# Kernel optimization log

Measured on AMD Instinct MI355X. Metric: run time of the kernel, lower is better.

The kernel has to match this reference:

```python
import jax, jax.numpy as jnp
import numpy as np
from functools import partial

V, H, B, T, L = 32000, 1024, 64, 64, 4
EOS = 2


def setup_inputs() -> dict:
    key = jax.random.key(0)
    ks = jax.random.split(key, 10)
    s = 1.0 / np.sqrt(H)
    return {
        "max_len": T,
        "tgt": jax.random.randint(ks[0], (B, T), 0, V),
        "h0": jax.random.normal(ks[1], (L, B, H), jnp.float32),
        "c0": jax.random.normal(ks[2], (L, B, H), jnp.float32),
        "embedding": jax.random.normal(ks[3], (V, H), jnp.float32) * s,
        "W_ih": jax.random.normal(ks[4], (L, 4 * H, H), jnp.float32) * s,
        "W_hh": jax.random.normal(ks[5], (L, 4 * H, H), jnp.float32) * s,
        "b_ih": jax.random.normal(ks[6], (L, 4 * H), jnp.float32) * s,
        "b_hh": jax.random.normal(ks[7], (L, 4 * H), jnp.float32) * s,
        "W_cls": jax.random.normal(ks[8], (V, H), jnp.float32) * s,
        "b_cls": jax.random.normal(ks[9], (V,), jnp.float32) * s,
    }


def _lstm_cell(x, h, c, Wi, Wh, bi, bh):
    # gates: [B, 4H] in torch order (i, f, g, o)
    g = x @ Wi.T + bi + h @ Wh.T + bh
    i, f, gg, o = jnp.split(g, 4, axis=-1)
    c2 = jax.nn.sigmoid(f) * c + jax.nn.sigmoid(i) * jnp.tanh(gg)
    h2 = jax.nn.sigmoid(o) * jnp.tanh(c2)
    return h2, c2


def reference(max_len, tgt, h0, c0, embedding, W_ih, W_hh, b_ih, b_hh, W_cls, b_cls):
    # step i>0 uses embedding of tgt[:, i-1].
    batch = tgt.shape[0]
    x0 = jnp.broadcast_to(embedding[EOS], (batch, embedding.shape[1]))
    tf_in = embedding[tgt[:, : max_len - 1]]              # [B, T-1, H]
    inputs = jnp.concatenate([x0[:, None, :], tf_in], axis=1)  # [B, T, H]
    inputs = jnp.swapaxes(inputs, 0, 1)                   # [T, B, H]

    def step(carry, x):
        h, c = carry  # each [L, B, H]
        hs, cs = [], []
        inp = x
        for l in range(L):  # 4 stacked LSTM cells, h of cell l feeds cell l+1
            hn, cn = _lstm_cell(inp, h[l], c[l], W_ih[l], W_hh[l], b_ih[l], b_hh[l])
            hs.append(hn)
            cs.append(cn)
            inp = hn
        h = jnp.stack(hs)
        c = jnp.stack(cs)
        logp = jax.nn.log_softmax(h[L - 1] @ W_cls.T + b_cls, axis=-1)  # [B, V]
        return (h, c), logp

    (h, c), out = jax.lax.scan(step, (h0, c0), inputs)
    return out, h, c  # out: [T, B, V]
```

## Files before the change

### kernel.cpp

```cpp
#include <hip/hip_runtime.h>

using u16 = unsigned short;
using u32 = unsigned int;

typedef __bf16 bf16x8 __attribute__((ext_vector_type(8)));
typedef float  f32x4  __attribute__((ext_vector_type(4)));
typedef u16    u16x8  __attribute__((ext_vector_type(8)));

static constexpr int kV = 32000, kH = 1024, kB = 64, kT = 64, kL = 4, kEOS = 2;

struct Flag { int v; int pad[15]; };

__device__ __forceinline__ u16 f2bf(float f) {
  u32 u = __float_as_uint(f);
  u = (u + 0x7fffu + ((u >> 16) & 1u)) >> 16;
  return (u16)u;
}
__device__ __forceinline__ float sigf(float x)   { return 1.0f / (1.0f + __expf(-x)); }
__device__ __forceinline__ float tanhf_(float x) { return 1.0f - 2.0f / (__expf(2.0f * x) + 1.0f); }

typedef const __attribute__((address_space(1))) u32* gas_ptr;
typedef __attribute__((address_space(3))) u32*       las_ptr;
__device__ __forceinline__ void async16(const u16* g, u16* l) {
  __builtin_amdgcn_global_load_lds((gas_ptr)g, (las_ptr)l, 16, 0, 0);
}

__device__ __forceinline__ void spin_ge(const int* p, int tgt) {
  while (__hip_atomic_load(p, __ATOMIC_RELAXED, __HIP_MEMORY_SCOPE_AGENT) < tgt)
    __builtin_amdgcn_s_sleep(2);
}

__device__ __forceinline__ size_t packed_off(int b, int k) {
  return (size_t)(((b >> 4) * 32 + (k >> 5)) * 512 + (((k >> 3) & 3) * 16 + (b & 15)) * 8 + (k & 7));
}

__device__ __forceinline__ u16x8 cvt8(const float* src) {
  const float4* s4 = (const float4*)src;
  float4 v0 = s4[0], v1 = s4[1];
  u16x8 r;
  r[0]=f2bf(v0.x); r[1]=f2bf(v0.y); r[2]=f2bf(v0.z); r[3]=f2bf(v0.w);
  r[4]=f2bf(v1.x); r[5]=f2bf(v1.y); r[6]=f2bf(v1.z); r[7]=f2bf(v1.w);
  return r;
}


__global__ void __launch_bounds__(256)
pack_lstm(const float* __restrict__ Wih, const float* __restrict__ Whh,
          u16* __restrict__ wpack) {
  __shared__ u16 lds[64 * 136];
  const int bid = blockIdx.x;
  const int lblk = bid >> 4, mt = (bid >> 3) & 1, kkg = bid & 7;
  const int lay = lblk >> 6, cb = lblk & 63;
  const int tid = threadIdx.x;
  const float* W = mt ? Whh : Wih;
  {
    const int rid = tid >> 2, q = tid & 3;
    const int gr = (rid >> 4) * 1024 + cb * 16 + (rid & 15);
    const float* src = W + ((size_t)lay * 4096 + gr) * 1024 + kkg * 128 + q * 32;
    u16* dst = lds + rid * 136 + q * 32;
    #pragma unroll
    for (int it = 0; it < 4; ++it)
      *(u16x8*)(dst + it * 8) = cvt8(src + it * 8);
  }
  __syncthreads();
  const int cf = tid >> 6, lane = tid & 63;
  const int rid = cf * 16 + (lane & 15);
  const int l4o = (lane >> 4) * 8;
  #pragma unroll
  for (int kl = 0; kl < 4; ++kl) {
    const int kk = kkg * 4 + kl;
    const u16x8 v = *(const u16x8*)(lds + rid * 136 + kl * 32 + l4o);
    *(u16x8*)(wpack + ((size_t)lblk * 16384 + mt * 8192 + kk * 256 + cf * 64 + lane) * 8) = v;
  }
}

__global__ void __launch_bounds__(256)
pack_cls(const float* __restrict__ W, u16* __restrict__ o) {
  __shared__ u16 lds[128 * 136];
  const int bid = blockIdx.x;
  const int bn = bid >> 3, kkg = bid & 7;
  const int tid = threadIdx.x;
  {
    const int row = tid >> 1, half = tid & 1;
    const float* src = W + ((size_t)(bn * 128 + row)) * 1024 + kkg * 128 + half * 64;
    u16* dst = lds + row * 136 + half * 64;
    #pragma unroll
    for (int it = 0; it < 8; ++it)
      *(u16x8*)(dst + it * 8) = cvt8(src + it * 8);
  }
  __syncthreads();
  #pragma unroll
  for (int kl = 0; kl < 4; ++kl) {
    const int kk = kkg * 4 + kl;
    #pragma unroll
    for (int q = 0; q < 2; ++q) {
      const int p = tid + q * 256, row = p & 127, l4 = p >> 7;
      const u16x8 v = *(const u16x8*)(lds + row * 136 + kl * 32 + l4 * 8);
      *(u16x8*)(o + ((size_t)bn * 16384 + kk * 512 + p) * 8) = v;
    }
  }
}

__global__ void pack_x(const float* __restrict__ emb, const int* __restrict__ tgt,
                       u16* __restrict__ X) {
  const int cid = blockIdx.x * 256 + threadIdx.x;
  const int kc = cid & 127, b = (cid >> 7) & 63, t = cid >> 13;
  const int tok = (t == 0) ? kEOS : tgt[b * 64 + t - 1];
  const u16x8 r = cvt8(emb + (size_t)tok * 1024 + kc * 8);
  *(u16x8*)(X + (size_t)t * 65536 + packed_off(b, kc * 8)) = r;
}

__global__ void pack_init(const float* __restrict__ h0, const float* __restrict__ bih,
                          const float* __restrict__ bhh, u16* __restrict__ hball,
                          float* __restrict__ bsum) {
  const int cid = blockIdx.x * 256 + threadIdx.x;
  if (cid < 32768) {
    const int kc = cid & 127, row = cid >> 7;
    const int lay = row >> 6, b = row & 63;
    const u16x8 r = cvt8(h0 + (size_t)cid * 8);
    *(u16x8*)(hball + (size_t)lay * 65 * 65536 + packed_off(b, kc * 8)) = r;
  } else {
    const int i = cid - 32768;
    bsum[i] = bih[i] + bhh[i];
  }
}

__global__ void __launch_bounds__(1024, 4)
lstm_coop(const u16* __restrict__ wpack, const u16* __restrict__ xall,
          u16* __restrict__ hball, const float* __restrict__ bsum,
          const float* __restrict__ c0, float* __restrict__ outh, float* __restrict__ outc,
          Flag* flags) {
  __shared__ u16 stg[3][32][512];
  __shared__ float Gc[2][64][80];

  const int tid = threadIdx.x, lane = tid & 63, wave = tid >> 6;
  const int l15 = lane & 15, l4 = lane >> 4;
  const int cmat = wave >> 3, cwc = (wave >> 1) & 3, ckh = wave & 1;
  const int blk = blockIdx.x;
  const int lay = (blk >> 1) & 3;
  const int cb  = ((blk >> 3) << 1) | (blk & 1);
  const int u0 = cb << 4;
  const int ub = tid >> 4, uu = tid & 15;

  float creg = c0[((size_t)lay * 64 + ub) * 1024 + u0 + uu];
  float bsv[4];
  #pragma unroll
  for (int g = 0; g < 4; ++g) bsv[g] = bsum[lay * 4096 + g * 1024 + u0 + uu];

  const size_t wbase = (size_t)(lay * 64 + cb) * 131072;
  bf16x8 breg[16];
  #pragma unroll
  for (int j = 0; j < 16; ++j)
    breg[j] = *(const bf16x8*)(wpack + wbase
        + (size_t)(((cmat * 32 + 2 * j + ckh) * 4) + cwc) * 512 + lane * 8);

  const int j0 = wave * 2, j1 = wave * 2 + 1;
  const int m2a = j0 >> 4, mta = (j0 >> 2) & 3, ksla = j0 & 3;
  const int m2b = j1 >> 4, mtb = (j1 >> 2) & 3, kslb = j1 & 3;

  u16* hlay = hball + (size_t)lay * 65 * 65536;
  const u16* hprev = (lay == 0) ? xall : (hball + (size_t)(lay - 1) * 65 * 65536);

  #pragma unroll 1
  for (int t = 0; t < kT; ++t) {
    if (t > 0 && tid < 64)                 spin_ge(&flags[lay * 64 + tid].v, t);
    if (lay > 0 && tid >= 64 && tid < 128) spin_ge(&flags[(lay - 1) * 64 + (tid - 64)].v, t + 1);
    __syncthreads();

    const u16* xsrc = (lay == 0) ? (xall + (size_t)t * 65536)
                                 : (hprev + (size_t)(t + 1) * 65536);
    const u16* hsrc = hlay + (size_t)t * 65536;

    const u16* ga = (m2a ? hsrc : xsrc) + (size_t)((mta * 32 + ksla) * 512) + lane * 8;
    const u16* gb = (m2b ? hsrc : xsrc) + (size_t)((mtb * 32 + kslb) * 512) + lane * 8;

    auto STAGE = [&](int c) {
      async16(ga + (size_t)c * 2048, &stg[c % 3][m2a * 16 + mta * 4 + ksla][0]);
      async16(gb + (size_t)c * 2048, &stg[c % 3][m2b * 16 + mtb * 4 + kslb][0]);
    };

    f32x4 acc[4] = {};
    STAGE(0); STAGE(1);
    #pragma unroll
    for (int c = 0; c < 8; ++c) {
      if (c < 7) asm volatile("s_waitcnt vmcnt(2)" ::: "memory");
      else       asm volatile("s_waitcnt vmcnt(0)" ::: "memory");
      __builtin_amdgcn_s_barrier();
      asm volatile("" ::: "memory");
      if (c < 6) STAGE(c + 2);
      const u16* As = &stg[c % 3][cmat * 16][0];
      __builtin_amdgcn_s_setprio(1);
      #pragma unroll
      for (int s = 0; s < 2; ++s) {
        const int ksl = 2 * s + ckh;
        bf16x8 a[4];
        #pragma unroll
        for (int m = 0; m < 4; ++m)
          a[m] = *(const bf16x8*)(As + (m * 4 + ksl) * 512 + lane * 8);
        #pragma unroll
        for (int m = 0; m < 4; ++m)
          acc[m] = __builtin_amdgcn_mfma_f32_16x16x32_bf16(a[m], breg[2 * c + s], acc[m], 0, 0, 0);
      }
      __builtin_amdgcn_s_setprio(0);
    }

    if (ckh == 0) {
      #pragma unroll
      for (int m = 0; m < 4; ++m)
        #pragma unroll
        for (int r = 0; r < 4; ++r)
          Gc[cmat][m * 16 + l4 * 4 + r][cwc * 16 + l15] = acc[m][r];
    }
    __syncthreads();
    if (ckh == 1) {
      #pragma unroll
      for (int m = 0; m < 4; ++m)
        #pragma unroll
        for (int r = 0; r < 4; ++r)
          Gc[cmat][m * 16 + l4 * 4 + r][cwc * 16 + l15] += acc[m][r];
    }
    __syncthreads();

    float sg[4];
    #pragma unroll
    for (int g = 0; g < 4; ++g) {
      const int col = g * 16 + uu;
      sg[g] = Gc[0][ub][col] + Gc[1][ub][col] + bsv[g];
    }
    const float c2 = sigf(sg[1]) * creg + sigf(sg[0]) * tanhf_(sg[2]);
    const float h2 = sigf(sg[3]) * tanhf_(c2);
    creg = c2;
    const u16 hv = f2bf(h2);
    if (t == kT - 1) {
      outh[((size_t)lay * 64 + ub) * 1024 + u0 + uu] = h2;
      outc[((size_t)lay * 64 + ub) * 1024 + u0 + uu] = c2;
    }
    const u32 other = __shfl_xor((u32)hv, 1);
    if ((tid & 1) == 0) {
      const u32 hpair = (u32)hv | (other << 16);
      u32* hdst = (u32*)(hlay + (size_t)(t + 1) * 65536 + packed_off(ub, u0 + uu));
      __hip_atomic_store(hdst, hpair, __ATOMIC_RELAXED, __HIP_MEMORY_SCOPE_AGENT);
    }
    __syncthreads();
    if (tid == 0)
      __hip_atomic_store(&flags[lay * 64 + cb].v, t + 1, __ATOMIC_RELAXED, __HIP_MEMORY_SCOPE_AGENT);
  }
}

__global__ void __launch_bounds__(512, 4)
cls_gemm(const u16* __restrict__ A, const u16* __restrict__ Bw,
         const float* __restrict__ bcls, float* __restrict__ out,
         float* __restrict__ pmax, float* __restrict__ psum) {
  __shared__ u16 sA[3][4096], sB[3][8192];
  const int tid = threadIdx.x, lane = tid & 63, wave = tid >> 6;
  const int wm = wave >> 2, wc = wave & 3;
  const int l15 = lane & 15, l4 = lane >> 4;
  const int bm = blockIdx.x, bny = blockIdx.y;
  const int bn0 = bny * 2;
  const u16* Ab = A + (size_t)bm * 131072;

  auto STAGE = [&](int kk) {
    u16* dA = sA[kk % 3]; u16* dB = sB[kk % 3];
    #pragma unroll
    for (int q = 0; q < 3; ++q) {
      const int c = wave * 3 + q;
      if (c < 8) {
        const u16* g = Ab + (size_t)(c >> 2) * 65536 + (size_t)(((c & 3) * 32 + kk) * 512) + lane * 8;
        async16(g, dA + c * 512);
      } else {
        const int b = c - 8, pan = b >> 3, v = b & 7;
        const u16* g = Bw + (size_t)(bn0 + pan) * 131072 + (size_t)kk * 4096 + v * 512 + lane * 8;
        async16(g, dB + pan * 4096 + v * 512);
      }
    }
  };

  f32x4 acc[4][4] = {};
  STAGE(0); STAGE(1);
  for (int kk = 0; kk < 32; ++kk) {
    if (kk < 31) asm volatile("s_waitcnt vmcnt(3)" ::: "memory");
    else         asm volatile("s_waitcnt vmcnt(0)" ::: "memory");
    __builtin_amdgcn_s_barrier();
    asm volatile("" ::: "memory");
    if (kk < 30) STAGE(kk + 2);
    const u16* aS = sA[kk % 3]; const u16* bS = sB[kk % 3];
    const int pan = wc >> 1, cbase = (wc & 1) * 64;
    bf16x8 av[4], bv[4];
    #pragma unroll
    for (int mi = 0; mi < 4; ++mi) av[mi] = *(const bf16x8*)(aS + (wm * 4 + mi) * 512 + lane * 8);
    #pragma unroll
    for (int ci = 0; ci < 4; ++ci)
      bv[ci] = *(const bf16x8*)(bS + pan * 4096 + l4 * 1024 + (cbase + ci * 16 + l15) * 8);
    #pragma unroll
    for (int mi = 0; mi < 4; ++mi)
      #pragma unroll
      for (int ci = 0; ci < 4; ++ci)
        acc[mi][ci] = __builtin_amdgcn_mfma_f32_16x16x32_bf16(av[mi], bv[ci], acc[mi][ci], 0, 0, 0);
  }
  float bc[4];
  #pragma unroll
  for (int ci = 0; ci < 4; ++ci) bc[ci] = bcls[bn0 * 128 + wc * 64 + ci * 16 + l15];
  u16* lb = (u16*)out;
  #pragma unroll
  for (int ci = 0; ci < 4; ++ci) {
    const int col = bn0 * 128 + wc * 64 + ci * 16 + l15;
    #pragma unroll
    for (int mi = 0; mi < 4; ++mi)
      #pragma unroll
      for (int r = 0; r < 4; ++r) {
        const int row = bm * 128 + wm * 64 + mi * 16 + l4 * 4 + r;
        const u16 v = f2bf(acc[mi][ci][r] + bc[ci]);
        const u32 other = __shfl_xor((u32)v, 1);
        if ((l15 & 1) == 0)
          *(u32*)(lb + (size_t)row * 64000 + col) = (u32)v | (other << 16);
      }
  }
  __syncthreads();
  {
    float* sRm = (float*)&sA[0][0];
    float* sRs = sRm + 512;
    #pragma unroll
    for (int mi = 0; mi < 4; ++mi) {
      #pragma unroll
      for (int r = 0; r < 4; ++r) {
        float v[4];
        #pragma unroll
        for (int ci = 0; ci < 4; ++ci) v[ci] = acc[mi][ci][r] + bc[ci];
        float mx = fmaxf(fmaxf(v[0], v[1]), fmaxf(v[2], v[3]));
        mx = fmaxf(mx, __shfl_xor(mx, 1)); mx = fmaxf(mx, __shfl_xor(mx, 2));
        mx = fmaxf(mx, __shfl_xor(mx, 4)); mx = fmaxf(mx, __shfl_xor(mx, 8));
        float ss = __expf(v[0]-mx) + __expf(v[1]-mx) + __expf(v[2]-mx) + __expf(v[3]-mx);
        ss += __shfl_xor(ss, 1); ss += __shfl_xor(ss, 2);
        ss += __shfl_xor(ss, 4); ss += __shfl_xor(ss, 8);
        const int lr = wm * 64 + mi * 16 + l4 * 4 + r;
        if (l15 == 0) { sRm[wc * 128 + lr] = mx; sRs[wc * 128 + lr] = ss; }
      }
    }
    __syncthreads();
    if (tid < 256) {
      const int pan = tid >> 7, row = tid & 127;
      const float m0 = sRm[(pan * 2) * 128 + row],     s0 = sRs[(pan * 2) * 128 + row];
      const float m1 = sRm[(pan * 2 + 1) * 128 + row], s1 = sRs[(pan * 2 + 1) * 128 + row];
      const float M = fmaxf(m0, m1);
      const float S = s0 * __expf(m0 - M) + s1 * __expf(m1 - M);
      pmax[(size_t)(bm * 128 + row) * 256 + (bn0 + pan)] = M;
      psum[(size_t)(bm * 128 + row) * 256 + (bn0 + pan)] = S;
    }
  }
}

__global__ void __launch_bounds__(256)
cls_gemm_f32(const u16* __restrict__ A, const float* __restrict__ Bw,
             const float* __restrict__ bcls, float* __restrict__ out,
             float* __restrict__ pmax, float* __restrict__ psum) {
  __shared__ u16 sA[3][4096], sB[3][4096];
  const int tid = threadIdx.x, lane = tid & 63, wave = tid >> 6;
  const int wm = wave >> 1, wc = wave & 1;
  const int l15 = lane & 15, l4 = lane >> 4;
  const int bm = blockIdx.x, bn = blockIdx.y;
  const u16*  Ab = A  + (size_t)bm * 131072;
  const float* Bb = Bw + (size_t)bn * 131072;

  auto LOADB = [&](int kk, u16x8* rb) {
    #pragma unroll
    for (int q = 0; q < 2; ++q) {
      const int p = tid + q * 256, row = p & 127, khi = p >> 7;
      rb[q] = cvt8(Bb + (size_t)row * 1024 + kk * 32 + khi * 8);
    }
  };
  auto WRITEB = [&](int kk, const u16x8* rb) {
    u16* dB = sB[kk % 3];
    #pragma unroll
    for (int q = 0; q < 2; ++q) {
      const int p = tid + q * 256, row = p & 127, khi = p >> 7;
      *(u16x8*)(dB + khi * 1024 + row * 8) = rb[q];
    }
  };
  auto STAGE_A = [&](int kk) {
    u16* dA = sA[kk % 3];
    #pragma unroll
    for (int q = 0; q < 2; ++q) {
      const int v = wave * 2 + q;
      const u16* g = Ab + (size_t)(v >> 2) * 65536 + (size_t)(((v & 3) * 32 + kk) * 512) + lane * 8;
      async16(g, dA + v * 512);
    }
  };

  f32x4 acc[4][4] = {};
  {
    u16x8 rb[2];
    LOADB(0, rb); STAGE_A(0); WRITEB(0, rb);
  }
  for (int kk = 0; kk < 32; ++kk) {
    if (kk < 31) {
      u16x8 rb[2];
      LOADB(kk + 1, rb);
      STAGE_A(kk + 1);
      WRITEB(kk + 1, rb);
    } else {
      asm volatile("s_waitcnt vmcnt(0)" ::: "memory");
    }
    __builtin_amdgcn_s_barrier();
    asm volatile("" ::: "memory");
    const u16* aS = sA[kk % 3]; const u16* bS = sB[kk % 3];
    bf16x8 av[4], bv[4];
    #pragma unroll
    for (int mi = 0; mi < 4; ++mi) av[mi] = *(const bf16x8*)(aS + (wm * 4 + mi) * 512 + lane * 8);
    #pragma unroll
    for (int ci = 0; ci < 4; ++ci) bv[ci] = *(const bf16x8*)(bS + l4 * 1024 + (wc * 64 + ci * 16 + l15) * 8);
    #pragma unroll
    for (int mi = 0; mi < 4; ++mi)
      #pragma unroll
      for (int ci = 0; ci < 4; ++ci)
        acc[mi][ci] = __builtin_amdgcn_mfma_f32_16x16x32_bf16(av[mi], bv[ci], acc[mi][ci], 0, 0, 0);
    asm volatile("" ::: "memory");
    __builtin_amdgcn_s_barrier();
  }
  float bc[4];
  #pragma unroll
  for (int ci = 0; ci < 4; ++ci) bc[ci] = bcls[bn * 128 + wc * 64 + ci * 16 + l15];
  u16* lb = (u16*)out;
  #pragma unroll
  for (int ci = 0; ci < 4; ++ci) {
    const int col = bn * 128 + wc * 64 + ci * 16 + l15;
    #pragma unroll
    for (int mi = 0; mi < 4; ++mi)
      #pragma unroll
      for (int r = 0; r < 4; ++r) {
        const int row = bm * 128 + wm * 64 + mi * 16 + l4 * 4 + r;
        const u16 v = f2bf(acc[mi][ci][r] + bc[ci]);
        const u32 other = __shfl_xor((u32)v, 1);
        if ((l15 & 1) == 0)
          *(u32*)(lb + (size_t)row * 64000 + col) = (u32)v | (other << 16);
      }
  }
  __syncthreads();
  {
    float* sRm = (float*)&sA[0][0];
    float* sRs = sRm + 256;
    #pragma unroll
    for (int mi = 0; mi < 4; ++mi) {
      #pragma unroll
      for (int r = 0; r < 4; ++r) {
        float v[4];
        #pragma unroll
        for (int ci = 0; ci < 4; ++ci) v[ci] = acc[mi][ci][r] + bc[ci];
        float mx = fmaxf(fmaxf(v[0], v[1]), fmaxf(v[2], v[3]));
        mx = fmaxf(mx, __shfl_xor(mx, 1)); mx = fmaxf(mx, __shfl_xor(mx, 2));
        mx = fmaxf(mx, __shfl_xor(mx, 4)); mx = fmaxf(mx, __shfl_xor(mx, 8));
        float ss = __expf(v[0]-mx) + __expf(v[1]-mx) + __expf(v[2]-mx) + __expf(v[3]-mx);
        ss += __shfl_xor(ss, 1); ss += __shfl_xor(ss, 2);
        ss += __shfl_xor(ss, 4); ss += __shfl_xor(ss, 8);
        const int lr = wm * 64 + mi * 16 + l4 * 4 + r;
        if (l15 == 0) { sRm[wc * 128 + lr] = mx; sRs[wc * 128 + lr] = ss; }
      }
    }
    __syncthreads();
    if (tid < 128) {
      const float m0 = sRm[tid], s0 = sRs[tid];
      const float m1 = sRm[128 + tid], s1 = sRs[128 + tid];
      const float M = fmaxf(m0, m1);
      const float S = s0 * __expf(m0 - M) + s1 * __expf(m1 - M);
      pmax[(size_t)(bm * 128 + tid) * 256 + bn] = M;
      psum[(size_t)(bm * 128 + tid) * 256 + bn] = S;
    }
  }
}

__global__ void __launch_bounds__(256)
lsm_sub(const float* __restrict__ pmax, const float* __restrict__ psum,
        float* __restrict__ out) {
  __shared__ float rm[256], rs[256];
  __shared__ u16 rowbuf[32000];
  const int r = blockIdx.x, b = threadIdx.x;
  const u16* lb = (const u16*)out;
  for (int j = b; j < 4000; j += 256)
    *(u16x8*)(rowbuf + j * 8) = *(const u16x8*)(lb + (size_t)r * 64000 + j * 8);
  float m = -3.0e38f, s = 0.0f;
  if (b < 250) { m = pmax[(size_t)r * 256 + b]; s = psum[(size_t)r * 256 + b]; }
  rm[b] = m; rs[b] = s; __syncthreads();
  for (int st = 128; st > 0; st >>= 1) {
    if (b < st) {
      const float m2 = rm[b + st], s2 = rs[b + st];
      const float M = fmaxf(rm[b], m2);
      rs[b] = rs[b] * __expf(rm[b] - M) + s2 * __expf(m2 - M);
      rm[b] = M;
    }
    __syncthreads();
  }
  const float z = rm[0] + logf(rs[0]);
  float* po = out + (size_t)r * 32000;
  for (int j = b; j < 4000; j += 256) {
    const u16x8 v = *(const u16x8*)(rowbuf + j * 8);
    float4 o0, o1;
    o0.x = __uint_as_float((u32)v[0] << 16) - z;
    o0.y = __uint_as_float((u32)v[1] << 16) - z;
    o0.z = __uint_as_float((u32)v[2] << 16) - z;
    o0.w = __uint_as_float((u32)v[3] << 16) - z;
    o1.x = __uint_as_float((u32)v[4] << 16) - z;
    o1.y = __uint_as_float((u32)v[5] << 16) - z;
    o1.z = __uint_as_float((u32)v[6] << 16) - z;
    o1.w = __uint_as_float((u32)v[7] << 16) - z;
    *(float4*)(po + j * 8)     = o0;
    *(float4*)(po + j * 8 + 4) = o1;
  }
}

extern "C" void kernel_launch(void* const* d_in, const int* in_sizes, int n_in,
                              void* d_out, int out_size, void* d_ws, size_t ws_size,
                              hipStream_t stream) {
  (void)in_sizes; (void)n_in; (void)out_size;
  const int*   tgt  = (const int*)d_in[1];
  const float* h0   = (const float*)d_in[2];
  const float* c0   = (const float*)d_in[3];
  const float* emb  = (const float*)d_in[4];
  const float* Wih  = (const float*)d_in[5];
  const float* Whh  = (const float*)d_in[6];
  const float* bih  = (const float*)d_in[7];
  const float* bhh  = (const float*)d_in[8];
  const float* Wcls = (const float*)d_in[9];
  const float* bcls = (const float*)d_in[10];

  float* out  = (float*)d_out;
  float* outh = out + (size_t)kT * kB * kV;
  float* outc = outh + (size_t)kL * kB * kH;

  const size_t SZ_WPACK = 67108864;
  const size_t SZ_WCLS  = 65536000;
  const size_t SZ_X     = 8388608;
  const size_t SZ_HBALL = 34078720;
  const size_t SZ_BSUM  = 65536;
  const size_t SZ_FLAGS = 16384;
  const size_t SZ_PM    = 4194304;
  const size_t FULL_REQ = SZ_WPACK + SZ_WCLS + SZ_X + SZ_HBALL + SZ_BSUM + SZ_FLAGS + 2 * SZ_PM;
  const bool full = (ws_size >= FULL_REQ);

  char* ws = (char*)d_ws;
  size_t off = 0;
  u16* wpack = (u16*)(ws + off); off += SZ_WPACK;
  u16* wclsb = nullptr;
  if (full) { wclsb = (u16*)(ws + off); off += SZ_WCLS; }
  u16*   X     = (u16*)(ws + off); off += SZ_X;
  u16*   hball = (u16*)(ws + off); off += SZ_HBALL;
  float* bsum  = (float*)(ws + off); off += SZ_BSUM;
  Flag*  flags = (Flag*)(ws + off);  off += SZ_FLAGS;
  float* pmax  = (float*)(ws + off); off += SZ_PM;
  float* psum  = (float*)(ws + off); off += SZ_PM;

  pack_lstm<<<4096, 256, 0, stream>>>(Wih, Whh, wpack);
  if (full) pack_cls<<<2000, 256, 0, stream>>>(Wcls, wclsb);
  pack_x   <<<2048,  256, 0, stream>>>(emb, tgt, X);
  pack_init<<<192,   256, 0, stream>>>(h0, bih, bhh, hball, bsum);
  hipMemsetAsync(flags, 0, SZ_FLAGS, stream);

  void* args[] = { (void*)&wpack, (void*)&X, (void*)&hball, (void*)&bsum,
                   (void*)&c0, (void*)&outh, (void*)&outc, (void*)&flags };
  hipLaunchCooperativeKernel((const void*)lstm_coop, dim3(256), dim3(1024), args, 0, stream);

  const u16* h3a = hball + (size_t)3 * 65 * 65536 + 65536;
  if (full) cls_gemm    <<<dim3(32, 125), 512, 0, stream>>>(h3a, wclsb, bcls, out, pmax, psum);
  else      cls_gemm_f32<<<dim3(32, 250), 256, 0, stream>>>(h3a, Wcls,  bcls, out, pmax, psum);
  lsm_sub<<<4096, 256, 0, stream>>>(pmax, psum, out);
}
```

Before: 1.188 ms.

## Deepen async staging to four buffers and reuse staging LDS for gate reduction

The per-step K loop now issues four async global-to-LDS chunk loads up front into a 4-deep staging buffer and processes two chunks per barrier. This halves the barrier count and keeps more loads in flight. The separate Gc reduction buffer is removed: each of the four wave groups writes its partial gates into the now-free staging LDS, and one barrier replaces the two-phase write-then-accumulate. A single 4-way sum then forms the gates. LDS footprint stays similar, and the risk lies in the wait counts and the reuse of staging memory after the last chunk.

New measurement: 1.254 ms. +5.6%, slower.

```diff
diff --git a/kernel.cpp b/kernel.cpp
--- a/kernel.cpp
+++ b/kernel.cpp
@@ -130,8 +130,7 @@
           u16* __restrict__ hball, const float* __restrict__ bsum,
           const float* __restrict__ c0, float* __restrict__ outh, float* __restrict__ outc,
           Flag* flags) {
-  __shared__ u16 stg[3][32][512];
-  __shared__ float Gc[2][64][80];
+  __shared__ u16 stg[4][32][512];
 
   const int tid = threadIdx.x, lane = tid & 63, wave = tid >> 6;
   const int l15 = lane & 15, l4 = lane >> 4;
@@ -175,57 +174,56 @@
     const u16* gb = (m2b ? hsrc : xsrc) + (size_t)((mtb * 32 + kslb) * 512) + lane * 8;
 
     auto STAGE = [&](int c) {
-      async16(ga + (size_t)c * 2048, &stg[c % 3][m2a * 16 + mta * 4 + ksla][0]);
-      async16(gb + (size_t)c * 2048, &stg[c % 3][m2b * 16 + mtb * 4 + kslb][0]);
+      async16(ga + (size_t)c * 2048, &stg[c & 3][m2a * 16 + mta * 4 + ksla][0]);
+      async16(gb + (size_t)c * 2048, &stg[c & 3][m2b * 16 + mtb * 4 + kslb][0]);
     };
 
     f32x4 acc[4] = {};
-    STAGE(0); STAGE(1);
-    #pragma unroll
-    for (int c = 0; c < 8; ++c) {
-      if (c < 7) asm volatile("s_waitcnt vmcnt(2)" ::: "memory");
-      else       asm volatile("s_waitcnt vmcnt(0)" ::: "memory");
+    STAGE(0); STAGE(1); STAGE(2); STAGE(3);
+    #pragma unroll
+    for (int i = 0; i < 4; ++i) {
+      if (i == 0) asm volatile("s_waitcnt vmcnt(4)" ::: "memory");
+      else        asm volatile("s_waitcnt vmcnt(0)" ::: "memory");
       __builtin_amdgcn_s_barrier();
       asm volatile("" ::: "memory");
-      if (c < 6) STAGE(c + 2);
-      const u16* As = &stg[c % 3][cmat * 16][0];
-      __builtin_amdgcn_s_setprio(1);
-      #pragma unroll
-      for (int s = 0; s < 2; ++s) {
-        const int ksl = 2 * s + ckh;
-        bf16x8 a[4];
+      if (i == 1)      { STAGE(4); STAGE(5); }
+      else if (i == 2) { STAGE(6); STAGE(7); }
+      #pragma unroll
+      for (int cc = 0; cc < 2; ++cc) {
+        const int c = 2 * i + cc;
+        const u16* As = &stg[c & 3][cmat * 16][0];
+        __builtin_amdgcn_s_setprio(1);
         #pragma unroll
-        for (int m = 0; m < 4; ++m)
-          a[m] = *(const bf16x8*)(As + (m * 4 + ksl) * 512 + lane * 8);
-        #pragma unroll
-        for (int m = 0; m < 4; ++m)
-          acc[m] = __builtin_amdgcn_mfma_f32_16x16x32_bf16(a[m], breg[2 * c + s], acc[m], 0, 0, 0);
+        for (int s = 0; s < 2; ++s) {
+          const int ksl = 2 * s + ckh;
+          bf16x8 a[4];
+          #pragma unroll
+          for (int m = 0; m < 4; ++m)
+            a[m] = *(const bf16x8*)(As + (m * 4 + ksl) * 512 + lane * 8);
+          #pragma unroll
+          for (int m = 0; m < 4; ++m)
+            acc[m] = __builtin_amdgcn_mfma_f32_16x16x32_bf16(a[m], breg[2 * c + s], acc[m], 0, 0, 0);
+        }
+        __builtin_amdgcn_s_setprio(0);
       }
-      __builtin_amdgcn_s_setprio(0);
-    }
-
-    if (ckh == 0) {
+    }
+
+    {
+      float* Gq = (float*)&stg[0][0][0] + (cmat * 2 + ckh) * 4096;
       #pragma unroll
       for (int m = 0; m < 4; ++m)
         #pragma unroll
         for (int r = 0; r < 4; ++r)
-          Gc[cmat][m * 16 + l4 * 4 + r][cwc * 16 + l15] = acc[m][r];
+          Gq[(m * 16 + l4 * 4 + r) * 64 + cwc * 16 + l15] = acc[m][r];
     }
     __syncthreads();
-    if (ckh == 1) {
-      #pragma unroll
-      for (int m = 0; m < 4; ++m)
-        #pragma unroll
-        for (int r = 0; r < 4; ++r)
-          Gc[cmat][m * 16 + l4 * 4 + r][cwc * 16 + l15] += acc[m][r];
-    }
-    __syncthreads();
-
+
+    const float* Gf = (const float*)&stg[0][0][0];
     float sg[4];
     #pragma unroll
     for (int g = 0; g < 4; ++g) {
-      const int col = g * 16 + uu;
-      sg[g] = Gc[0][ub][col] + Gc[1][ub][col] + bsv[g];
+      const int idx = ub * 64 + g * 16 + uu;
+      sg[g] = Gf[idx] + Gf[4096 + idx] + Gf[8192 + idx] + Gf[12288 + idx] + bsv[g];
     }
     const float c2 = sigf(sg[1]) * creg + sigf(sg[0]) * tanhf_(sg[2]);
     const float h2 = sigf(sg[3]) * tanhf_(c2);
```
